# Performance work log

Hardware: AMD Instinct MI355X
Metric: run time of the kernel (lower is better)

## Reference

```python
import jax, jax.numpy as jnp
import numpy as np

NUM_BASES = 8
DEGREE = 3
KSIZE = 3
DOMAIN = (0.0, 1.0)


def bspline_basis(x, degree, knots):
    """Cox-de Boor recursion, vectorized over all elements of x.
    x: [...] float; knots: [num_bases + degree + 1].
    Returns basis values of shape [..., num_bases].
    (The original torch code evaluates this same recursion per-tap inside
    nested loops; here it is evaluated once, batched, with correct knot
    index bookkeeping. Uniform distinct knots -> no zero denominators.)
    """
    xe = x[..., None]  # [..., 1]
    # degree-0: indicator of each knot interval -> [..., L-1]
    B = ((knots[:-1] <= xe) & (xe < knots[1:])).astype(x.dtype)
    for d in range(1, degree + 1):
        left = (xe - knots[:-(d + 1)]) / (knots[d:-1] - knots[:-(d + 1)]) * B[..., :-1]
        right = (knots[d + 1:] - xe) / (knots[d + 1:] - knots[1:-d]) * B[..., 1:]
        B = left + right  # [..., L-d-1]
    return B  # [..., num_bases]


def setup_inputs() -> dict:
    key = jax.random.key(0)
    k1, k2 = jax.random.split(key)
    # inputs uniform in [0,1) so they lie inside the B-spline domain
    x = jax.random.uniform(k1, (16, 64, 64, 64), dtype=jnp.float32)
    # per-tap spline coefficients: [Cout, Cin, K, K, num_bases]
    coeff = jax.random.normal(k2, (64, 64, KSIZE, KSIZE, NUM_BASES), dtype=jnp.float32)
    return {"x": x, "coeff": coeff}


def reference(x, coeff):
    # normalize to domain (identity for domain=(0,1), kept for faithfulness)
    xn = (x - DOMAIN[0]) / (DOMAIN[1] - DOMAIN[0])
    knots = jnp.linspace(DOMAIN[0], DOMAIN[1], NUM_BASES + DEGREE + 1, dtype=x.dtype)
    # spline basis for every input element: [B, Cin, H, W, nb]
    phi = bspline_basis(xn, DEGREE, knots)
    Bn, Cin, H, W, nb = phi.shape
    Cout = coeff.shape[0]
    # The KAN conv  out[b,o,h,w] = sum_{j,k,l,m} phi[b,j,h+k,w+l,m]*coeff[o,j,k,l,m]
    # is exactly a VALID conv with Cin*nb input channels.
    phi_c = jnp.transpose(phi, (0, 1, 4, 2, 3)).reshape(Bn, Cin * nb, H, W)
    w = jnp.transpose(coeff, (0, 1, 4, 2, 3)).reshape(Cout, Cin * nb, KSIZE, KSIZE)
    out = jax.lax.conv_general_dilated(
        phi_c, w, window_strides=(1, 1), padding="VALID",
        dimension_numbers=("NCHW", "OIHW", "NCHW"))
    return out  # [B, Cout, H-K+1, W-K+1]
```

## Files before the change

### kernel.cpp

```cpp
#include <hip/hip_runtime.h>
#include <hip/hip_bf16.h>


typedef short v8s __attribute__((ext_vector_type(8)));
typedef float v4f __attribute__((ext_vector_type(4)));
typedef float v16f __attribute__((ext_vector_type(16)));
typedef unsigned long long u64;
typedef u64 v2u64 __attribute__((ext_vector_type(2)));

#define B_N   16
#define CIN   64
#define COUT  64
#define H_IN  64
#define W_IN  64
#define NB    8
#define HO    62
#define WO    62
#define JC    8
#define NCH   8

__device__ __forceinline__ ushort f2bf(float f) {
    uint xu = __float_as_uint(f);
    return (ushort)((xu + 0x7fffu + ((xu >> 16) & 1u)) >> 16);
}

__device__ __forceinline__ uint cvtpk(float a, float b) {
    uint r;
    asm("v_cvt_pk_bf16_f32 %0, %1, %2" : "=v"(r) : "v"(a), "v"(b));
    return r;
}

__global__ void prep_coeff_kernel(const float* __restrict__ coeff, ushort* __restrict__ bt) {
    int n = blockIdx.x * 256 + threadIdx.x;
    if (n >= 294912) return;
    int m  = n & 7;
    int g2 = (n >> 3) & 1;
    int o  = (n >> 4) & 63;
    int jp = (n >> 10) & 3;
    int q  = n >> 12;
    int tap = q % 9;
    int jc  = q / 9;
    int j = jc * 8 + jp * 2 + g2;
    bt[n] = f2bf(coeff[((o * CIN + j) * 9 + tap) * 8 + m]);
}

#define MFMA32(a, b, c) __builtin_amdgcn_mfma_f32_32x32x16_bf16((a), (b), (c), 0, 0, 0)
#define MFMA16(a, b, c) __builtin_amdgcn_mfma_f32_16x16x32_bf16((a), (b), (c), 0, 0, 0)

__global__ __launch_bounds__(256, 5) void kan_conv_os(
        const float* __restrict__ x, const ushort* __restrict__ cb,
        float* __restrict__ out) {
    const int h    = blockIdx.x;
    const int b    = blockIdx.y;
    const int obh  = blockIdx.z;
    const int tid  = threadIdx.x;
    const int lane = tid & 63;
    const int kh   = tid >> 6;
    const int l31  = lane & 31;
    const int g2   = lane >> 5;

    __shared__ __align__(16) char smraw[24576];

    char* wrB = smraw + kh * 6144 + lane * 16;
    const char* rdB = smraw + kh * 6144 + g2 * 1024 + l31 * 16;

    v16f c0 = (v16f)(0.f), c1 = (v16f)(0.f);

    float xr[6];
    const float* xb = x + ((size_t)(b * CIN) * H_IN + h) * W_IN + lane;
    const int jx = kh * 2;

#define XL(dst, jcn) { \
    _Pragma("unroll") \
    for (int e = 0; e < 6; ++e) \
        dst[e] = xb[(size_t)((jcn) * 8 + jx + (e & 1)) * (H_IN * W_IN) + (e >> 1) * W_IN]; \
    }

    auto PW = [&](float xval, int e) {
        float s_ = fminf(fmaxf(xval * 11.0f, 0.0f), 10.999f);
        int i0 = (int)s_;
        float u  = s_ - (float)i0;
        float t  = 1.0f - u;
        float u2 = u * u, u3 = u2 * u;
        float t3 = t * t * t;
        const float inv6 = 1.0f / 6.0f;
        float n0 = t3 * inv6;
        float n3 = u3 * inv6;
        float n1 = fmaf(u2, fmaf(u, 0.5f, -1.0f), 2.0f / 3.0f);
        float n2 = 1.0f - n0 - n1 - n3;
        u64 V = (u64)cvtpk(n0, n1) | ((u64)cvtpk(n2, n3) << 32);
        int bi = i0 - 3;
        u64 lo = bi < 0 ? (V >> (uint)(-16 * bi))
               : bi < 4 ? (V << (uint)(16 * bi)) : 0ull;
        u64 hi = bi <= 0 ? 0ull
               : bi < 4 ? (V >> (uint)(64 - 16 * bi))
               : (V << (uint)(16 * bi - 64));
        v2u64 pk; pk[0] = lo; pk[1] = hi;
        *reinterpret_cast<v2u64*>(wrB + e * 1024) = pk;
    };

    const char* pA = (const char*)cb + (size_t)(kh * 128 + obh * 64 + l31 * 2 + g2) * 16;

    v8s aA, aB, aC;

#define TAPR(k, lt, C, N, nptr) { \
    v8s b0 = *reinterpret_cast<const v8s*>(rdB + (k) * 2048 + (lt) * 16); \
    v8s b1 = *reinterpret_cast<const v8s*>(rdB + (k) * 2048 + 512 + (lt) * 16); \
    N = *reinterpret_cast<const v8s*>(nptr); \
    c0 = MFMA32(C, b0, c0); \
    c1 = MFMA32(C, b1, c1); }

#define CHUNKP(jc) { \
    const char* pAc = pA + (size_t)(jc) * 73728; \
    const char* pAn = pA + (size_t)(((jc) + 1 < NCH) ? (jc) + 1 : 0) * 73728; \
    if ((jc) + 1 < NCH) XL(xr, (jc) + 1); \
    TAPR(0, 0, aA, aC, pAc + 2 * 8192); \
    TAPR(0, 1, aB, aA, pAc + 3 * 8192); \
    TAPR(0, 2, aC, aB, pAc + 4 * 8192); \
    if ((jc) + 1 < NCH) { PW(xr[0], 0); PW(xr[1], 1); } \
    TAPR(1, 0, aA, aC, pAc + 5 * 8192); \
    TAPR(1, 1, aB, aA, pAc + 6 * 8192); \
    TAPR(1, 2, aC, aB, pAc + 7 * 8192); \
    if ((jc) + 1 < NCH) { PW(xr[2], 2); PW(xr[3], 3); } \
    TAPR(2, 0, aA, aC, pAc + 8 * 8192); \
    TAPR(2, 1, aB, aA, pAn + 0 * 8192); \
    TAPR(2, 2, aC, aB, pAn + 1 * 8192); \
    if ((jc) + 1 < NCH) { PW(xr[4], 4); PW(xr[5], 5); } \
    }

    XL(xr, 0);
    aA = *reinterpret_cast<const v8s*>(pA);
    aB = *reinterpret_cast<const v8s*>(pA + 8192);
    PW(xr[0], 0); PW(xr[1], 1); PW(xr[2], 2);
    PW(xr[3], 3); PW(xr[4], 4); PW(xr[5], 5);

    CHUNKP(0); CHUNKP(1); CHUNKP(2); CHUNKP(3);
    CHUNKP(4); CHUNKP(5); CHUNKP(6); CHUNKP(7);

#define WR1(C, off) { \
    _Pragma("unroll") \
    for (int q = 0; q < 4; ++q) { \
        v4f v; \
        _Pragma("unroll") \
        for (int z = 0; z < 4; ++z) v[z] = C[q * 4 + z]; \
        *reinterpret_cast<v4f*>(smraw + (off) + q * 1024 + lane * 16) = v; \
    } }
#define ADD1(C, off) { \
    _Pragma("unroll") \
    for (int q = 0; q < 4; ++q) { \
        v4f v = *reinterpret_cast<const v4f*>(smraw + (off) + q * 1024 + lane * 16); \
        _Pragma("unroll") \
        for (int z = 0; z < 4; ++z) C[q * 4 + z] += v[z]; \
    } }
#define STORE1(C, WF) { \
    int w = (WF) * 32 + l31; \
    if (w < WO) { \
        _Pragma("unroll") \
        for (int reg = 0; reg < 16; ++reg) { \
            int o = obh * 32 + (reg & 3) + 8 * (reg >> 2) + 4 * g2; \
            out[((b * COUT + o) * HO + h) * WO + w] = C[reg]; \
        } } }

    __syncthreads();
    if (kh == 1) { WR1(c0, 0);     WR1(c1, 4096); }
    if (kh == 3) { WR1(c0, 8192);  WR1(c1, 12288); }
    __syncthreads();
    if (kh == 0) { ADD1(c0, 0);    ADD1(c1, 4096); }
    if (kh == 2) { ADD1(c0, 8192); ADD1(c1, 12288); }
    __syncthreads();
    if (kh == 2) WR1(c0, 16384);
    if (kh == 0) WR1(c1, 20480);
    __syncthreads();
    if (kh == 0) { ADD1(c0, 16384); STORE1(c0, 0); }
    if (kh == 2) { ADD1(c1, 20480); STORE1(c1, 1); }
}

__global__ __launch_bounds__(256, 4) void kan_conv_fb(
        const float* __restrict__ x, const float* __restrict__ coeff_f,
        float* __restrict__ out) {
    const int h    = blockIdx.x;
    const int b    = blockIdx.y;
    const int tid  = threadIdx.x;
    const int lane = tid & 63;
    const int wv   = tid >> 6;
    const int g    = lane >> 4;
    const int l15  = lane & 15;
    const int obase = (wv >> 1) << 5;
    const int wbase = (wv & 1) << 5;

    __shared__ __align__(16) ushort phi_lds[3 * JC * W_IN * NB];
    __shared__ uint lut[72];
    if (tid < 72) {
        int tap = tid;
        int j  = tap / 9;
        int r9 = tap - j * 9;
        int kt = r9 / 3;
        int lt = r9 - kt * 3;
        lut[tap] = (uint)(((kt * JC + j) * W_IN) * NB) | ((uint)lt << 16)
                 | ((uint)j << 20) | ((uint)r9 << 24);
    }
    v4f acc00 = {0.f, 0.f, 0.f, 0.f};
    v4f acc01 = acc00, acc10 = acc00, acc11 = acc00;
    const int aoff = obase + l15;
    float xv[6];
    #pragma unroll
    for (int it = 0; it < 6; ++it) {
        int n = it * 256 + tid;
        xv[it] = x[((b * CIN + ((n >> 6) & 7)) * H_IN + (h + (n >> 9))) * W_IN + (n & 63)];
    }
    for (int jc = 0; jc < NCH; ++jc) {
        #pragma unroll
        for (int it = 0; it < 6; ++it) {
            int n = it * 256 + tid;
            float s  = xv[it] * 11.0f;
            int i0 = (int)s;
            i0 = i0 < 0 ? 0 : (i0 > 10 ? 10 : i0);
            float u  = s - (float)i0;
            float um = 1.0f - u;
            float u2 = u * u, u3 = u2 * u;
            const float inv6 = 1.0f / 6.0f;
            float n0 = um * um * um * inv6;
            float n1 = (3.0f * u3 - 6.0f * u2 + 4.0f) * inv6;
            float n2 = (-3.0f * u3 + 3.0f * u2 + 3.0f * u + 1.0f) * inv6;
            float n3 = u3 * inv6;
            u64 V = (u64)f2bf(n0) | ((u64)f2bf(n1) << 16)
                  | ((u64)f2bf(n2) << 32) | ((u64)f2bf(n3) << 48);
            int bi = i0 - 3;
            u64 lo = bi < 0 ? (V >> (uint)(-16 * bi))
                   : bi < 4 ? (V << (uint)(16 * bi)) : 0ull;
            u64 hi = bi <= 0 ? 0ull
                   : bi < 4 ? (V >> (uint)(64 - 16 * bi))
                   : (V << (uint)(16 * bi - 64));
            v2u64 pk; pk[0] = lo; pk[1] = hi;
            *reinterpret_cast<v2u64*>(&phi_lds[n << 3]) = pk;
        }
        if (jc + 1 < NCH) {
            int j0n = (jc + 1) * JC;
            #pragma unroll
            for (int it = 0; it < 6; ++it) {
                int n = it * 256 + tid;
                xv[it] = x[((b * CIN + j0n + ((n >> 6) & 7)) * H_IN + (h + (n >> 9))) * W_IN + (n & 63)];
            }
        }
        __syncthreads();
        const int j0 = jc * JC;
        #pragma unroll 6
        for (int kk = 0; kk < 18; ++kk) {
            int tap = (kk << 2) + g;
            uint e = lut[tap];
            int philoc = (int)(e & 0xffffu);
            int lt     = (int)((e >> 16) & 3u);
            int w0 = wbase + l15 + lt;
            int w1 = w0 + 16;
            w0 = w0 < 63 ? w0 : 63;
            w1 = w1 < 63 ? w1 : 63;
            v8s pb0 = *reinterpret_cast<const v8s*>(&phi_lds[philoc + (w0 << 3)]);
            v8s pb1 = *reinterpret_cast<const v8s*>(&phi_lds[philoc + (w1 << 3)]);
            int j  = (int)((e >> 20) & 15u);
            int r9 = (int)((e >> 24) & 15u);
            const float* cf = coeff_f + (((aoff * CIN + (j0 + j)) * 9 + r9) << 3);
            v8s pa0, pa1;
            #pragma unroll
            for (int z = 0; z < 8; ++z) pa0[z] = (short)f2bf(cf[z]);
            const float* cf2 = cf + (CIN * 9 * NB * 16);
            #pragma unroll
            for (int z = 0; z < 8; ++z) pa1[z] = (short)f2bf(cf2[z]);
            acc00 = MFMA16(pa0, pb0, acc00);
            acc01 = MFMA16(pa0, pb1, acc01);
            acc10 = MFMA16(pa1, pb0, acc10);
            acc11 = MFMA16(pa1, pb1, acc11);
        }
        __syncthreads();
    }
    const int wc0 = wbase + l15;
    const int wc1 = wc0 + 16;
    #pragma unroll
    for (int i = 0; i < 2; ++i) {
        v4f a0 = (i == 0) ? acc00 : acc10;
        v4f a1 = (i == 0) ? acc01 : acc11;
        int o = obase + i * 16 + (g << 2);
        #pragma unroll
        for (int r = 0; r < 4; ++r) {
            int off = ((b * COUT + o + r) * HO + h) * WO;
            if (wc0 < WO) out[off + wc0] = a0[r];
            if (wc1 < WO) out[off + wc1] = a1[r];
        }
    }
}

extern "C" void kernel_launch(void* const* d_in, const int* in_sizes, int n_in,
                              void* d_out, int out_size, void* d_ws, size_t ws_size,
                              hipStream_t stream) {
    const float* x     = (const float*)d_in[0];
    const float* coeff = (const float*)d_in[1];
    float* out = (float*)d_out;

    const size_t bt_bytes = (size_t)294912 * 2;
    if (ws_size >= bt_bytes) {
        ushort* bt = (ushort*)d_ws;
        prep_coeff_kernel<<<(294912 + 255) / 256, 256, 0, stream>>>(coeff, bt);
        kan_conv_os<<<dim3(HO, B_N, 2), 256, 0, stream>>>(x, bt, out);
    } else {
        kan_conv_fb<<<dim3(HO, B_N), 256, 0, stream>>>(x, coeff, out);
    }
}
```

Measured before the change: 59.42 us.

## Merge output-channel halves into one 512-thread block with double-buffered basis LDS

The two output-channel halves, formerly separate blocks, now run as eight waves in one block. They share a single basis-function tile in LDS, so each block computes phi once instead of twice. The basis LDS is double-buffered across Cin chunks, and the next chunk's phi is computed and written while the MFMAs of the current chunk run, with one barrier per chunk. The A/B register loads are software-pipelined more finely in even/odd stages. In exchange, LDS per block doubles, barriers are block-wide each chunk, and the grid has half as many blocks.

```diff
diff --git a/kernel.cpp b/kernel.cpp
--- a/kernel.cpp
+++ b/kernel.cpp
@@ -47,36 +47,39 @@
 #define MFMA32(a, b, c) __builtin_amdgcn_mfma_f32_32x32x16_bf16((a), (b), (c), 0, 0, 0)
 #define MFMA16(a, b, c) __builtin_amdgcn_mfma_f32_16x16x32_bf16((a), (b), (c), 0, 0, 0)
 
-__global__ __launch_bounds__(256, 5) void kan_conv_os(
+__global__ __launch_bounds__(512, 4) void kan_conv_dr(
         const float* __restrict__ x, const ushort* __restrict__ cb,
         float* __restrict__ out) {
     const int h    = blockIdx.x;
     const int b    = blockIdx.y;
-    const int obh  = blockIdx.z;
     const int tid  = threadIdx.x;
     const int lane = tid & 63;
-    const int kh   = tid >> 6;
+    const int wv   = tid >> 6;
+    const int kh   = wv & 3;
+    const int oh   = wv >> 2;
     const int l31  = lane & 31;
     const int g2   = lane >> 5;
 
-    __shared__ __align__(16) char smraw[24576];
-
-    char* wrB = smraw + kh * 6144 + lane * 16;
-    const char* rdB = smraw + kh * 6144 + g2 * 1024 + l31 * 16;
+    __shared__ __align__(16) char smraw[49408];
+
+    char* const wrBb = smraw + kh * 6144 + lane * 16;
+    const char* const rdBb = smraw + kh * 6144 + g2 * 1024 + l31 * 16;
 
     v16f c0 = (v16f)(0.f), c1 = (v16f)(0.f);
 
-    float xr[6];
+    float xr[3];
+    const int jx  = kh * 2;
+    const int eo0 = oh * 3;
     const float* xb = x + ((size_t)(b * CIN) * H_IN + h) * W_IN + lane;
-    const int jx = kh * 2;
-
-#define XL(dst, jcn) { \
+
+#define XL3(jcn) { \
     _Pragma("unroll") \
-    for (int e = 0; e < 6; ++e) \
-        dst[e] = xb[(size_t)((jcn) * 8 + jx + (e & 1)) * (H_IN * W_IN) + (e >> 1) * W_IN]; \
-    }
-
-    auto PW = [&](float xval, int e) {
+    for (int i = 0; i < 3; ++i) { \
+        int e_ = eo0 + i; \
+        xr[i] = xb[(size_t)((jcn) * 8 + jx + (e_ & 1)) * (H_IN * W_IN) + (e_ >> 1) * W_IN]; \
+    } }
+
+    auto PW = [&](float xval, int e, char* wb) {
         float s_ = fminf(fmaxf(xval * 11.0f, 0.0f), 10.999f);
         int i0 = (int)s_;
         float u  = s_ - (float)i0;
@@ -96,46 +99,61 @@
                : bi < 4 ? (V >> (uint)(64 - 16 * bi))
                : (V << (uint)(16 * bi - 64));
         v2u64 pk; pk[0] = lo; pk[1] = hi;
-        *reinterpret_cast<v2u64*>(wrB + e * 1024) = pk;
+        *reinterpret_cast<v2u64*>(wb + e * 1024) = pk;
     };
 
-    const char* pA = (const char*)cb + (size_t)(kh * 128 + obh * 64 + l31 * 2 + g2) * 16;
+    const char* pA = (const char*)cb + (size_t)(kh * 128 + oh * 64 + l31 * 2 + g2) * 16;
 
     v8s aA, aB, aC;
-
-#define TAPR(k, lt, C, N, nptr) { \
-    v8s b0 = *reinterpret_cast<const v8s*>(rdB + (k) * 2048 + (lt) * 16); \
-    v8s b1 = *reinterpret_cast<const v8s*>(rdB + (k) * 2048 + 512 + (lt) * 16); \
-    N = *reinterpret_cast<const v8s*>(nptr); \
-    c0 = MFMA32(C, b0, c0); \
-    c1 = MFMA32(C, b1, c1); }
-
-#define CHUNKP(jc) { \
+    v8s bE0, bE1, bO0, bO1;
+
+#define CHUNKX(jc) { \
     const char* pAc = pA + (size_t)(jc) * 73728; \
-    const char* pAn = pA + (size_t)(((jc) + 1 < NCH) ? (jc) + 1 : 0) * 73728; \
-    if ((jc) + 1 < NCH) XL(xr, (jc) + 1); \
-    TAPR(0, 0, aA, aC, pAc + 2 * 8192); \
-    TAPR(0, 1, aB, aA, pAc + 3 * 8192); \
-    TAPR(0, 2, aC, aB, pAc + 4 * 8192); \
-    if ((jc) + 1 < NCH) { PW(xr[0], 0); PW(xr[1], 1); } \
-    TAPR(1, 0, aA, aC, pAc + 5 * 8192); \
-    TAPR(1, 1, aB, aA, pAc + 6 * 8192); \
-    TAPR(1, 2, aC, aB, pAc + 7 * 8192); \
-    if ((jc) + 1 < NCH) { PW(xr[2], 2); PW(xr[3], 3); } \
-    TAPR(2, 0, aA, aC, pAc + 8 * 8192); \
-    TAPR(2, 1, aB, aA, pAn + 0 * 8192); \
-    TAPR(2, 2, aC, aB, pAn + 1 * 8192); \
-    if ((jc) + 1 < NCH) { PW(xr[4], 4); PW(xr[5], 5); } \
-    }
-
-    XL(xr, 0);
-    aA = *reinterpret_cast<const v8s*>(pA);
-    aB = *reinterpret_cast<const v8s*>(pA + 8192);
-    PW(xr[0], 0); PW(xr[1], 1); PW(xr[2], 2);
-    PW(xr[3], 3); PW(xr[4], 4); PW(xr[5], 5);
-
-    CHUNKP(0); CHUNKP(1); CHUNKP(2); CHUNKP(3);
-    CHUNKP(4); CHUNKP(5); CHUNKP(6); CHUNKP(7);
+    const char* pAn = pA + (size_t)(((jc) + 1) & 7) * 73728; \
+    const char* rb  = rdBb + ((jc) & 1) * 24576; \
+    char* wb        = wrBb + (((jc) + 1) & 1) * 24576; \
+    bE0 = *(const v8s*)(rb);                  bE1 = *(const v8s*)(rb + 512); \
+    if ((jc) + 1 < NCH) XL3((jc) + 1); \
+     aC = *(const v8s*)(pAc + 16384); \
+        bO0 = *(const v8s*)(rb + 16);         bO1 = *(const v8s*)(rb + 528); \
+        c0 = MFMA32(aA, bE0, c0);             c1 = MFMA32(aA, bE1, c1); \
+     aA = *(const v8s*)(pAc + 24576); \
+        bE0 = *(const v8s*)(rb + 32);         bE1 = *(const v8s*)(rb + 544); \
+        c0 = MFMA32(aB, bO0, c0);             c1 = MFMA32(aB, bO1, c1); \
+     aB = *(const v8s*)(pAc + 32768); \
+        bO0 = *(const v8s*)(rb + 2048);       bO1 = *(const v8s*)(rb + 2560); \
+        c0 = MFMA32(aC, bE0, c0);             c1 = MFMA32(aC, bE1, c1); \
+     aC = *(const v8s*)(pAc + 40960); \
+        bE0 = *(const v8s*)(rb + 2064);       bE1 = *(const v8s*)(rb + 2576); \
+        c0 = MFMA32(aA, bO0, c0);             c1 = MFMA32(aA, bO1, c1); \
+     aA = *(const v8s*)(pAc + 49152); \
+        bO0 = *(const v8s*)(rb + 2080);       bO1 = *(const v8s*)(rb + 2592); \
+        c0 = MFMA32(aB, bE0, c0);             c1 = MFMA32(aB, bE1, c1); \
+    if ((jc) + 1 < NCH) PW(xr[0], eo0, wb); \
+     aB = *(const v8s*)(pAc + 57344); \
+        bE0 = *(const v8s*)(rb + 4096);       bE1 = *(const v8s*)(rb + 4608); \
+        c0 = MFMA32(aC, bO0, c0);             c1 = MFMA32(aC, bO1, c1); \
+     aC = *(const v8s*)(pAc + 65536); \
+        bO0 = *(const v8s*)(rb + 4112);       bO1 = *(const v8s*)(rb + 4624); \
+        c0 = MFMA32(aA, bE0, c0);             c1 = MFMA32(aA, bE1, c1); \
+    if ((jc) + 1 < NCH) PW(xr[1], eo0 + 1, wb); \
+     aA = *(const v8s*)(pAn); \
+        bE0 = *(const v8s*)(rb + 4128);       bE1 = *(const v8s*)(rb + 4640); \
+        c0 = MFMA32(aB, bO0, c0);             c1 = MFMA32(aB, bO1, c1); \
+     aB = *(const v8s*)(pAn + 8192); \
+        c0 = MFMA32(aC, bE0, c0);             c1 = MFMA32(aC, bE1, c1); \
+    if ((jc) + 1 < NCH) PW(xr[2], eo0 + 2, wb); \
+    __syncthreads(); \
+    }
+
+    XL3(0);
+    aA = *(const v8s*)(pA);
+    aB = *(const v8s*)(pA + 8192);
+    PW(xr[0], eo0, wrBb); PW(xr[1], eo0 + 1, wrBb); PW(xr[2], eo0 + 2, wrBb);
+    __syncthreads();
+
+    CHUNKX(0); CHUNKX(1); CHUNKX(2); CHUNKX(3);
+    CHUNKX(4); CHUNKX(5); CHUNKX(6); CHUNKX(7);
 
 #define WR1(C, off) { \
     _Pragma("unroll") \
@@ -157,22 +175,23 @@
     if (w < WO) { \
         _Pragma("unroll") \
         for (int reg = 0; reg < 16; ++reg) { \
-            int o = obh * 32 + (reg & 3) + 8 * (reg >> 2) + 4 * g2; \
+            int o = oh * 32 + (reg & 3) + 8 * (reg >> 2) + 4 * g2; \
             out[((b * COUT + o) * HO + h) * WO + w] = C[reg]; \
         } } }
 
-    __syncthreads();
-    if (kh == 1) { WR1(c0, 0);     WR1(c1, 4096); }
-    if (kh == 3) { WR1(c0, 8192);  WR1(c1, 12288); }
-    __syncthreads();
-    if (kh == 0) { ADD1(c0, 0);    ADD1(c1, 4096); }
-    if (kh == 2) { ADD1(c0, 8192); ADD1(c1, 12288); }
-    __syncthreads();
-    if (kh == 2) WR1(c0, 16384);
-    if (kh == 0) WR1(c1, 20480);
-    __syncthreads();
-    if (kh == 0) { ADD1(c0, 16384); STORE1(c0, 0); }
-    if (kh == 2) { ADD1(c1, 20480); STORE1(c1, 1); }
+    const int ro = oh * 16384;
+    __syncthreads();
+    if (kh == 1) { WR1(c0, ro);        WR1(c1, ro + 4096); }
+    if (kh == 3) { WR1(c0, ro + 8192); WR1(c1, ro + 12288); }
+    __syncthreads();
+    if (kh == 0) { ADD1(c0, ro);        ADD1(c1, ro + 4096); }
+    if (kh == 2) { ADD1(c0, ro + 8192); ADD1(c1, ro + 12288); }
+    __syncthreads();
+    if (kh == 2) WR1(c0, ro);
+    if (kh == 0) WR1(c1, ro + 4096);
+    __syncthreads();
+    if (kh == 0) { ADD1(c0, ro);        STORE1(c0, 0); }
+    if (kh == 2) { ADD1(c1, ro + 4096); STORE1(c1, 1); }
 }
 
 __global__ __launch_bounds__(256, 4) void kan_conv_fb(
@@ -299,7 +318,7 @@
     if (ws_size >= bt_bytes) {
         ushort* bt = (ushort*)d_ws;
         prep_coeff_kernel<<<(294912 + 255) / 256, 256, 0, stream>>>(coeff, bt);
-        kan_conv_os<<<dim3(HO, B_N, 2), 256, 0, stream>>>(x, bt, out);
+        kan_conv_dr<<<dim3(HO, B_N), 512, 0, stream>>>(x, bt, out);
     } else {
         kan_conv_fb<<<dim3(HO, B_N), 256, 0, stream>>>(x, coeff, out);
     }
```

New measurement: 54.43 us. 1.09x faster.
